# Kernel tuning notes

Hardware: AMD Instinct MI355X
Metric: run time of the kernel (lower is better)

The kernel has to match this reference:

```python
import jax, jax.numpy as jnp
import numpy as np

LN_EPS = 1e-5

def layer_norm(x, gamma, beta):
    mu = jnp.mean(x, axis=-1, keepdims=True)
    var = jnp.mean(jnp.square(x - mu), axis=-1, keepdims=True)
    return (x - mu) * jax.lax.rsqrt(var + LN_EPS) * gamma + beta

def setup_inputs() -> dict:
    key = jax.random.key(0)
    ks = jax.random.split(key, 16)
    B, S, E, D, H, F = 4, 2048, 768, 768, 12, 3072
    dh = D // H
    sc = lambda fan_in: 1.0 / np.sqrt(fan_in)
    x = jax.random.normal(ks[0], (B, S, E), dtype=jnp.float32)
    mask = jax.random.randint(ks[1], (B, S, S), 0, 2) > 0
    # per-head projection weights, torch Linear layout [out, in]
    Wq = jax.random.uniform(ks[2], (H, dh, E), minval=-sc(E), maxval=sc(E))
    bq = jax.random.uniform(ks[3], (H, dh), minval=-sc(E), maxval=sc(E))
    Wk = jax.random.uniform(ks[4], (H, dh, E), minval=-sc(E), maxval=sc(E))
    bk = jax.random.uniform(ks[5], (H, dh), minval=-sc(E), maxval=sc(E))
    Wv = jax.random.uniform(ks[6], (H, dh, E), minval=-sc(E), maxval=sc(E))
    bv = jax.random.uniform(ks[7], (H, dh), minval=-sc(E), maxval=sc(E))
    gamma = jnp.ones((D,), dtype=jnp.float32)
    beta = jnp.zeros((D,), dtype=jnp.float32)
    W1 = jax.random.uniform(ks[8], (F, D), minval=-sc(D), maxval=sc(D))
    b1 = jax.random.uniform(ks[9], (F,), minval=-sc(D), maxval=sc(D))
    W2 = jax.random.uniform(ks[10], (D, F), minval=-sc(F), maxval=sc(F))
    b2 = jax.random.uniform(ks[11], (D,), minval=-sc(F), maxval=sc(F))
    return {"x": x, "mask": mask, "Wq": Wq, "bq": bq, "Wk": Wk, "bk": bk,
            "Wv": Wv, "bv": bv, "gamma": gamma, "beta": beta,
            "W1": W1, "b1": b1, "W2": W2, "b2": b2}

def reference(x, mask, Wq, bq, Wk, bk, Wv, bv, gamma, beta, W1, b1, W2, b2):
    B, S, E = x.shape
    # per-head projections, vectorized over heads: [B,H,S,dh]
    q = jnp.einsum('bse,hde->bhsd', x, Wq) + bq[None, :, None, :]
    k = jnp.einsum('bse,hde->bhsd', x, Wk) + bk[None, :, None, :]
    v = jnp.einsum('bse,hde->bhsd', x, Wv) + bv[None, :, None, :]
    # NOTE: original scales by len(q[0])**0.5 == sqrt(seq_len), not sqrt(d_head)
    scores = jnp.einsum('bhsd,bhtd->bhst', q, k) / jnp.sqrt(jnp.asarray(S, x.dtype))
    scores = jnp.where(mask[:, None, :, :], jnp.asarray(-1000.0, x.dtype), scores)
    # NOTE: original softmax is over dim=1 of [B,Sq,Sk] => the QUERY axis (axis 2 here)
    attn = jax.nn.softmax(scores, axis=2)
    o = jnp.einsum('bhst,bhtd->bhsd', attn, v)  # [B,H,S,dh]
    a = jnp.transpose(o, (0, 2, 1, 3)).reshape(B, S, -1)  # concat heads -> [B,S,D]
    a = layer_norm(a, gamma, beta) + a
    h = jax.nn.relu(jnp.einsum('bsd,fd->bsf', a, W1) + b1)
    b = jnp.einsum('bsf,df->bsd', h, W2) + b2
    b = layer_norm(b, gamma, beta) + b
    return b
```

## Files before the change

kernel.cpp:

```cpp
#include <hip/hip_runtime.h>
#include <hip/hip_bf16.h>
#include <stdint.h>

using bf16 = __hip_bfloat16;
typedef __attribute__((ext_vector_type(8))) short short8;
typedef __attribute__((ext_vector_type(4))) short short4v;
typedef __attribute__((ext_vector_type(4))) float f32x4;

#define MFMA16(a, b, c) __builtin_amdgcn_mfma_f32_16x16x32_bf16((a), (b), (c), 0, 0, 0)

#if __has_builtin(__builtin_amdgcn_mfma_f32_16x16x16bf16_1k)
#define MFMAK16(a, b, c) __builtin_amdgcn_mfma_f32_16x16x16bf16_1k((a), (b), (c), 0, 0, 0)
#elif __has_builtin(__builtin_amdgcn_mfma_f32_16x16x16_bf16_1k)
#define MFMAK16(a, b, c) __builtin_amdgcn_mfma_f32_16x16x16_bf16_1k((a), (b), (c), 0, 0, 0)
#elif __has_builtin(__builtin_amdgcn_mfma_f32_16x16x16_bf16)
#define MFMAK16(a, b, c) __builtin_amdgcn_mfma_f32_16x16x16_bf16((a), (b), (c), 0, 0, 0)
#else
static __device__ __forceinline__ f32x4 mfmak16_asm(short4v a, short4v b, f32x4 c) {
  f32x4 d;
  asm("v_mfma_f32_16x16x16_bf16 %0, %1, %2, %3" : "=v"(d) : "v"(a), "v"(b), "v"(c));
  return d;
}
#define MFMAK16(a, b, c) mfmak16_asm((a), (b), (c))
#endif

static constexpr float SCLE = 0.031879358f;

__device__ __forceinline__ void g2l16(const void* g, void* l) {
  __builtin_amdgcn_global_load_lds((const __attribute__((address_space(1))) void*)g,
                                   (__attribute__((address_space(3))) void*)l, 16, 0, 0);
}

__device__ __forceinline__ short8 frag(const bf16* lds, int row, int slot) {
  return *(const short8*)((const char*)lds + row * 128 + (((slot ^ (row & 7)) & 7) << 4));
}

__global__ __launch_bounds__(256) void cvt_kernel(const float* __restrict__ in,
                                                  bf16* __restrict__ out, int n8) {
  int i = blockIdx.x * 256 + threadIdx.x;
  if (i >= n8) return;
  float4 f0 = ((const float4*)in)[i * 2 + 0];
  float4 f1 = ((const float4*)in)[i * 2 + 1];
  bf16 t[8] = {__float2bfloat16(f0.x), __float2bfloat16(f0.y),
               __float2bfloat16(f0.z), __float2bfloat16(f0.w),
               __float2bfloat16(f1.x), __float2bfloat16(f1.y),
               __float2bfloat16(f1.z), __float2bfloat16(f1.w)};
  ((float4*)out)[i] = *(const float4*)t;
}

__global__ void detect_kernel(const int* __restrict__ m, int* __restrict__ flag) {
  int v = m[threadIdx.x];
  unsigned long long ok = __ballot((v == 0) || (v == 1));
  if (threadIdx.x == 0) *flag = (ok == 0xFFFFFFFFFFFFFFFFULL) ? 1 : 0;
}

__global__ __launch_bounds__(256) void pack_kernel(const void* __restrict__ maskp,
                                                   const int* __restrict__ flagp,
                                                   uint32_t* __restrict__ pm) {
  const int i = blockIdx.x * 256 + threadIdx.x;
  uint32_t nib;
  if (*flagp) {
    const int4 v = ((const int4*)maskp)[i];
    nib = (v.x != 0) | ((v.y != 0) << 1) | ((v.z != 0) << 2) | ((v.w != 0) << 3);
  } else {
    const uchar4 c = ((const uchar4*)maskp)[i];
    nib = (c.x != 0) | ((c.y != 0) << 1) | ((c.z != 0) << 2) | ((c.w != 0) << 3);
  }
  uint32_t w = nib << ((i & 7) * 4);
  w |= __shfl_xor(w, 1, 64);
  w |= __shfl_xor(w, 2, 64);
  w |= __shfl_xor(w, 4, 64);
  if ((threadIdx.x & 7) == 0) pm[i >> 3] = w;
}

template <int EPI>
__global__ __launch_bounds__(256) void gemm_bt_kernel(
    const bf16* __restrict__ A, const bf16* __restrict__ Bm, int N, int K,
    const float* __restrict__ bias0, const float* __restrict__ bias1,
    const float* __restrict__ bias2, void* __restrict__ outp) {
  __shared__ bf16 aLds[2][128 * 32];
  __shared__ bf16 bLds[2][128 * 32];
  const int tid = threadIdx.x;
  const int wave = tid >> 6, lane = tid & 63;
  const int l15 = lane & 15, l4 = lane >> 4;
  const int row0 = blockIdx.y << 7, col0 = blockIdx.x << 7;
  const int wm = (wave >> 1) << 6, wn = (wave & 1) << 6;

  f32x4 acc[4][4] = {};

  const int sr = tid >> 2;
  const int sc = (tid & 3) << 3;
  const bf16* ga = A + (size_t)(row0 + sr) * K + sc;
  const bf16* gb = Bm + (size_t)(col0 + sr) * K + sc;
  const size_t rK64 = (size_t)64 * K;

  auto stage = [&](int buf, int k0) {
    g2l16(ga + k0, &aLds[buf][wave * 512]);
    g2l16(ga + k0 + rK64, &aLds[buf][2048 + wave * 512]);
    g2l16(gb + k0, &bLds[buf][wave * 512]);
    g2l16(gb + k0 + rK64, &bLds[buf][2048 + wave * 512]);
  };

  stage(0, 0);
  __syncthreads();
  const int NT = K >> 5;
  for (int t = 0; t < NT; t++) {
    if (t + 1 < NT) stage((t + 1) & 1, (t + 1) << 5);
    const bf16* la = aLds[t & 1];
    const bf16* lb = bLds[t & 1];
    short8 af[4], bfr[4];
#pragma unroll
    for (int i = 0; i < 4; i++)
      af[i] = *(const short8*)&la[(wm + i * 16 + l15) * 32 + l4 * 8];
#pragma unroll
    for (int i = 0; i < 4; i++)
      bfr[i] = *(const short8*)&lb[(wn + i * 16 + l15) * 32 + l4 * 8];
#pragma unroll
    for (int i = 0; i < 4; i++)
#pragma unroll
      for (int j = 0; j < 4; j++) acc[i][j] = MFMA16(af[i], bfr[j], acc[i][j]);
    __syncthreads();
  }

  if (EPI == 0) {
#pragma unroll
    for (int j = 0; j < 4; j++) {
      const int gcol = col0 + wn + j * 16 + l15;
      const int which = gcol / 768;
      const int oo = gcol - which * 768;
      const float* bs = (which == 0) ? bias0 : ((which == 1) ? bias1 : bias2);
      const float bv = bs[oo];
      const int h = oo >> 6, d = oo & 63;
      if (which < 2) {
        const float scl = (which == 0) ? SCLE : 1.0f;
        bf16* outb = (bf16*)outp + (size_t)which * 6291456;
#pragma unroll
        for (int i = 0; i < 4; i++) {
#pragma unroll
          for (int r = 0; r < 4; r++) {
            const int grow = row0 + wm + i * 16 + l4 * 4 + r;
            const int b = grow >> 11, s = grow & 2047;
            outb[((size_t)((b * 12 + h) * 2048 + s)) * 64 + d] =
                __float2bfloat16((acc[i][j][r] + bv) * scl);
          }
        }
      } else {
        bf16* vt = (bf16*)outp + (size_t)2 * 6291456;
#pragma unroll
        for (int i = 0; i < 4; i++) {
          const int grow = row0 + wm + i * 16 + l4 * 4;
          const int b = grow >> 11, s = grow & 2047;
          bf16 t4[4];
#pragma unroll
          for (int r = 0; r < 4; r++) t4[r] = __float2bfloat16(acc[i][j][r] + bv);
          *(short4v*)&vt[((size_t)((b * 12 + h) * 64 + d)) * 2048 + s] =
              *(const short4v*)t4;
        }
      }
    }
  } else if (EPI == 1) {
    bf16* outb = (bf16*)outp;
#pragma unroll
    for (int j = 0; j < 4; j++) {
      const int gcol = col0 + wn + j * 16 + l15;
      const float bv = bias0[gcol];
#pragma unroll
      for (int i = 0; i < 4; i++)
#pragma unroll
        for (int r = 0; r < 4; r++) {
          const int grow = row0 + wm + i * 16 + l4 * 4 + r;
          float v = acc[i][j][r] + bv;
          v = v > 0.f ? v : 0.f;
          outb[(size_t)grow * N + gcol] = __float2bfloat16(v);
        }
    }
  } else {
    float* outf = (float*)outp;
#pragma unroll
    for (int j = 0; j < 4; j++) {
      const int gcol = col0 + wn + j * 16 + l15;
      const float bv = bias0[gcol];
#pragma unroll
      for (int i = 0; i < 4; i++)
#pragma unroll
        for (int r = 0; r < 4; r++) {
          const int grow = row0 + wm + i * 16 + l4 * 4 + r;
          outf[(size_t)grow * N + gcol] = acc[i][j][r] + bv;
        }
    }
  }
}

__global__ __launch_bounds__(256) void gemm_bt64_kernel(
    const bf16* __restrict__ A, const bf16* __restrict__ Bm, int N, int K,
    const float* __restrict__ bias0, float* __restrict__ outf) {
  __shared__ bf16 aLds[2][64 * 32];
  __shared__ bf16 bLds[2][128 * 32];
  const int tid = threadIdx.x;
  const int wave = tid >> 6, lane = tid & 63;
  const int l15 = lane & 15, l4 = lane >> 4;
  const int row0 = blockIdx.y << 6, col0 = blockIdx.x << 7;
  const int wm = (wave >> 1) << 5, wn = (wave & 1) << 6;

  f32x4 acc[2][4] = {};

  const int sr = tid >> 2;
  const int sc = (tid & 3) << 3;
  const bf16* ga = A + (size_t)(row0 + sr) * K + sc;
  const bf16* gb = Bm + (size_t)(col0 + sr) * K + sc;
  const size_t rK64 = (size_t)64 * K;

  auto stage = [&](int buf, int k0) {
    g2l16(ga + k0, &aLds[buf][wave * 512]);
    g2l16(gb + k0, &bLds[buf][wave * 512]);
    g2l16(gb + k0 + rK64, &bLds[buf][2048 + wave * 512]);
  };

  stage(0, 0);
  __syncthreads();
  const int NT = K >> 5;
  for (int t = 0; t < NT; t++) {
    if (t + 1 < NT) stage((t + 1) & 1, (t + 1) << 5);
    const bf16* la = aLds[t & 1];
    const bf16* lb = bLds[t & 1];
    short8 af[2], bfr[4];
#pragma unroll
    for (int i = 0; i < 2; i++)
      af[i] = *(const short8*)&la[(wm + i * 16 + l15) * 32 + l4 * 8];
#pragma unroll
    for (int j = 0; j < 4; j++)
      bfr[j] = *(const short8*)&lb[(wn + j * 16 + l15) * 32 + l4 * 8];
#pragma unroll
    for (int i = 0; i < 2; i++)
#pragma unroll
      for (int j = 0; j < 4; j++) acc[i][j] = MFMA16(af[i], bfr[j], acc[i][j]);
    __syncthreads();
  }

#pragma unroll
  for (int j = 0; j < 4; j++) {
    const int gcol = col0 + wn + j * 16 + l15;
    const float bv = bias0[gcol];
#pragma unroll
    for (int i = 0; i < 2; i++)
#pragma unroll
      for (int r = 0; r < 4; r++) {
        const int grow = row0 + wm + i * 16 + l4 * 4 + r;
        outf[(size_t)grow * N + gcol] = acc[i][j][r] + bv;
      }
  }
}

__global__ __launch_bounds__(256) void zsum_kernel(
    const bf16* __restrict__ Qb, const bf16* __restrict__ Kb,
    const uint32_t* __restrict__ pm, bf16* __restrict__ Vt) {
  __shared__ bf16 qLds[2][64 * 64];
  __shared__ float zbuf[64];
  const int tid = threadIdx.x, wave = tid >> 6, lane = tid & 63;
  const int l15 = lane & 15, l4 = lane >> 4;
  const int srr = lane >> 3, sss = lane & 7;
  const int bid = blockIdx.x;
  const int swz = (bid & 7) * 192 + (bid >> 3);
  const int bh = swz >> 5, ttile = swz & 31;
  const int b = bh / 12;
  const int t0 = (ttile << 6) + (wave << 4);
  const size_t qkBase = (size_t)bh * (2048 * 64);
  const bf16* Kp = Kb + qkBase;
  const bf16* Qp = Qb + qkBase;
  const uint32_t* pmB = pm + (size_t)b * 2048 * 64;
  const int widx = t0 >> 5;
  const int shft = (wave & 1) * 16 + l4 * 4;

  short8 ak[2];
#pragma unroll
  for (int kc = 0; kc < 2; kc++)
    ak[kc] = *(const short8*)(Kp + (size_t)(t0 + l15) * 64 + kc * 32 + l4 * 8);

  auto stageQ = [&](int buf, int s0) {
#pragma unroll
    for (int p = 0; p < 2; p++) {
      const int r = p * 32 + wave * 8 + srr;
      g2l16(Qp + (size_t)(s0 + r) * 64 + ((sss ^ (r & 7)) << 3),
            &qLds[buf][p * 2048 + wave * 512]);
    }
  };

  f32x4 z = {};
  stageQ(0, 0);
  __syncthreads();

  for (int i = 0; i < 32; i++) {
    const int s0 = i << 6;
    if (i < 31) stageQ((i + 1) & 1, s0 + 64);
    const bf16* qb = qLds[i & 1];
    uint32_t mw[4];
#pragma unroll
    for (int sf = 0; sf < 4; sf++)
      mw[sf] = pmB[(size_t)(s0 + sf * 16 + l15) * 64 + widx];
#pragma unroll
    for (int sf = 0; sf < 4; sf++) {
      const short8 q0 = frag(qb, sf * 16 + l15, l4);
      const short8 q1 = frag(qb, sf * 16 + l15, 4 + l4);
      __builtin_amdgcn_s_setprio(1);
      f32x4 cc = {};
      cc = MFMA16(ak[0], q0, cc);
      cc = MFMA16(ak[1], q1, cc);
      __builtin_amdgcn_s_setprio(0);
      const uint32_t bits = mw[sf] >> shft;
#pragma unroll
      for (int r = 0; r < 4; r++) {
        const float e = __builtin_amdgcn_exp2f(cc[r]);
        z[r] += ((bits >> r) & 1) ? 0.f : e;
      }
    }
    __syncthreads();
  }

#pragma unroll
  for (int r = 0; r < 4; r++) {
    float zz = z[r];
    zz += __shfl_xor(zz, 1, 64);
    zz += __shfl_xor(zz, 2, 64);
    zz += __shfl_xor(zz, 4, 64);
    zz += __shfl_xor(zz, 8, 64);
    if (l15 == 0) zbuf[(wave << 4) + (l4 << 2) + r] = 1.0f / zz;
  }
  __syncthreads();

  const int t0blk = ttile << 6;
  const int drow = tid >> 2;
  const int tcol = (tid & 3) << 4;
  bf16* vp = Vt + (size_t)bh * (64 * 2048) + (size_t)drow * 2048 + t0blk + tcol;
  bf16 v[16];
  *(short8*)&v[0] = *(const short8*)vp;
  *(short8*)&v[8] = *(const short8*)(vp + 8);
#pragma unroll
  for (int j = 0; j < 16; j++)
    v[j] = __float2bfloat16(__bfloat162float(v[j]) * zbuf[tcol + j]);
  *(short8*)vp = *(const short8*)&v[0];
  *(short8*)(vp + 8) = *(const short8*)&v[8];
}

__global__ __launch_bounds__(256, 4) void attn_pv_kernel(
    const bf16* __restrict__ Qb, const bf16* __restrict__ Kb,
    const bf16* __restrict__ Vt, const uint32_t* __restrict__ pm,
    float* __restrict__ aOut) {
  __shared__ bf16 kLds[2][64 * 64];
  __shared__ bf16 vLds[2][64 * 64];
  const int tid = threadIdx.x, wave = tid >> 6, lane = tid & 63;
  const int l15 = lane & 15, l4 = lane >> 4;
  const int srr = lane >> 3, sss = lane & 7;
  const int bid = blockIdx.x;
  const int swz = (bid & 7) * 96 + (bid >> 3);
  const int bh = swz >> 4, stile = swz & 15;
  const int b = bh / 12, h = bh - b * 12;
  const int s0 = (stile << 7) + (wave << 5);
  const size_t qkBase = (size_t)bh * (2048 * 64);
  const bf16* Kp = Kb + qkBase;
  const bf16* Qp = Qb + qkBase;
  const bf16* Vp = Vt + (size_t)bh * 64 * 2048;
  const uint32_t* pmB = pm + (size_t)b * 2048 * 64;

  auto stageKV = [&](int buf, int t0) {
#pragma unroll
    for (int p = 0; p < 2; p++) {
      const int r = p * 32 + wave * 8 + srr;
      g2l16(Kp + (size_t)(t0 + r) * 64 + ((sss ^ (r & 7)) << 3),
            &kLds[buf][p * 2048 + wave * 512]);
      g2l16(Vp + (size_t)r * 2048 + t0 + ((sss ^ (r & 7)) << 3),
            &vLds[buf][p * 2048 + wave * 512]);
    }
  };

  short8 qf[2][2];
#pragma unroll
  for (int mf = 0; mf < 2; mf++)
#pragma unroll
    for (int kc = 0; kc < 2; kc++)
      qf[mf][kc] = *(const short8*)(Qp + (size_t)(s0 + mf * 16 + l15) * 64 +
                                    kc * 32 + l4 * 8);

  f32x4 oacc[2][4] = {};
  stageKV(0, 0);
  __syncthreads();

  for (int i = 0; i < 32; i++) {
    const int t0 = i << 6;
    if (i < 31) stageKV((i + 1) & 1, t0 + 64);
    const bf16* kb = kLds[i & 1];
    const bf16* vb = vLds[i & 1];
    uint2 mw[2];
#pragma unroll
    for (int mf = 0; mf < 2; mf++)
      mw[mf] = *(const uint2*)(pmB + (size_t)(s0 + mf * 16 + l15) * 64 + (t0 >> 5));

#pragma unroll
    for (int tf = 0; tf < 4; tf++) {
      const int trow = tf * 16 + l15;
      const short8 a0 = frag(kb, trow, l4);
      const short8 a1 = frag(kb, trow, 4 + l4);
      short4v pa[2];
#pragma unroll
      for (int mf = 0; mf < 2; mf++) {
        __builtin_amdgcn_s_setprio(1);
        f32x4 cc = {};
        cc = MFMA16(a0, qf[mf][0], cc);
        cc = MFMA16(a1, qf[mf][1], cc);
        __builtin_amdgcn_s_setprio(0);
        const uint32_t bits =
            ((tf < 2) ? mw[mf].x : mw[mf].y) >> ((tf & 1) * 16 + l4 * 4);
        bf16 p4[4];
#pragma unroll
        for (int r = 0; r < 4; r++) {
          const float e = __builtin_amdgcn_exp2f(cc[r]);
          p4[r] = __float2bfloat16(((bits >> r) & 1) ? 0.f : e);
        }
        pa[mf] = *(const short4v*)p4;
      }
      __builtin_amdgcn_s_setprio(1);
#pragma unroll
      for (int nf = 0; nf < 4; nf++) {
        const int vrow = nf * 16 + l15;
        const short4v bv = *(const short4v*)(
            (const char*)vb + vrow * 128 +
            ((((tf * 2 + (l4 >> 1)) ^ (vrow & 7)) & 7) << 4) + (l4 & 1) * 8);
        oacc[0][nf] = MFMAK16(pa[0], bv, oacc[0][nf]);
        oacc[1][nf] = MFMAK16(pa[1], bv, oacc[1][nf]);
      }
      __builtin_amdgcn_s_setprio(0);
    }
    __syncthreads();
  }

#pragma unroll
  for (int mf = 0; mf < 2; mf++)
#pragma unroll
    for (int nf = 0; nf < 4; nf++)
#pragma unroll
      for (int r = 0; r < 4; r++) {
        const int sg = s0 + mf * 16 + l4 * 4 + r;
        const int d = nf * 16 + l15;
        aOut[((size_t)(b * 2048 + sg)) * 768 + h * 64 + d] = oacc[mf][nf][r];
      }
}

template <int OUTMODE>
__global__ __launch_bounds__(256) void ln_kernel(const float* __restrict__ in,
                                                 const float* __restrict__ gamma,
                                                 const float* __restrict__ beta,
                                                 void* __restrict__ outp) {
  const int row = blockIdx.x, tid = threadIdx.x;
  const float* x = in + (size_t)row * 768;
  float v0 = x[tid], v1 = x[tid + 256], v2 = x[tid + 512];
  float s = v0 + v1 + v2;
#pragma unroll
  for (int m = 32; m >= 1; m >>= 1) s += __shfl_xor(s, m, 64);
  __shared__ float red[4];
  if ((tid & 63) == 0) red[tid >> 6] = s;
  __syncthreads();
  s = red[0] + red[1] + red[2] + red[3];
  const float mu = s * (1.f / 768.f);
  const float d0 = v0 - mu, d1 = v1 - mu, d2 = v2 - mu;
  float q = d0 * d0 + d1 * d1 + d2 * d2;
#pragma unroll
  for (int m = 32; m >= 1; m >>= 1) q += __shfl_xor(q, m, 64);
  __syncthreads();
  if ((tid & 63) == 0) red[tid >> 6] = q;
  __syncthreads();
  q = red[0] + red[1] + red[2] + red[3];
  const float rs = rsqrtf(q * (1.f / 768.f) + 1e-5f);
  const float y0 = d0 * rs * gamma[tid] + beta[tid] + v0;
  const float y1 = d1 * rs * gamma[tid + 256] + beta[tid + 256] + v1;
  const float y2 = d2 * rs * gamma[tid + 512] + beta[tid + 512] + v2;
  if (OUTMODE == 0) {
    float* o = (float*)outp + (size_t)row * 768;
    o[tid] = y0; o[tid + 256] = y1; o[tid + 512] = y2;
  } else {
    bf16* o = (bf16*)outp + (size_t)row * 768;
    o[tid] = __float2bfloat16(y0);
    o[tid + 256] = __float2bfloat16(y1);
    o[tid + 512] = __float2bfloat16(y2);
  }
}

extern "C" void kernel_launch(void* const* d_in, const int* in_sizes, int n_in,
                              void* d_out, int out_size, void* d_ws, size_t ws_size,
                              hipStream_t stream) {
  const float* x = (const float*)d_in[0];
  const void* mask = d_in[1];
  const float* Wq = (const float*)d_in[2];
  const float* bq = (const float*)d_in[3];
  const float* Wk = (const float*)d_in[4];
  const float* bk = (const float*)d_in[5];
  const float* Wv = (const float*)d_in[6];
  const float* bv = (const float*)d_in[7];
  const float* gamma = (const float*)d_in[8];
  const float* beta = (const float*)d_in[9];
  const float* W1 = (const float*)d_in[10];
  const float* b1 = (const float*)d_in[11];
  const float* W2 = (const float*)d_in[12];
  const float* b2 = (const float*)d_in[13];
  float* out = (float*)d_out;

  char* ws = (char*)d_ws;
  size_t o = 0;
  auto al = [&](size_t n) { size_t r = o; o = (o + n + 255) & ~(size_t)255; return r; };
  const size_t Q_off = al(12582912);
  const size_t K_off = al(12582912);
  const size_t V_off = al(12582912);
  const size_t XB_off = al(12582912);
  const size_t WQKV_off = al(3538944);
  const size_t H_off = Q_off;
  const size_t W1B_off = al(4718592);
  const size_t W2B_off = al(4718592);
  const size_t A_off = al(25165824);
  const size_t BF_off = A_off;
  const size_t A2_off = al(12582912);
  const size_t FL_off = al(256);
  const size_t PM_off = al(2097152);
  if (o > ws_size) return;

  bf16* Qb = (bf16*)(ws + Q_off);
  bf16* Kb = (bf16*)(ws + K_off);
  bf16* Vt = (bf16*)(ws + V_off);
  bf16* XB = (bf16*)(ws + XB_off);
  bf16* WQKV = (bf16*)(ws + WQKV_off);
  bf16* Hb = (bf16*)(ws + H_off);
  bf16* W1B = (bf16*)(ws + W1B_off);
  bf16* W2B = (bf16*)(ws + W2B_off);
  float* Af = (float*)(ws + A_off);
  float* Bf = (float*)(ws + BF_off);
  bf16* A2b = (bf16*)(ws + A2_off);
  int* flag = (int*)(ws + FL_off);
  uint32_t* pm = (uint32_t*)(ws + PM_off);

  cvt_kernel<<<3072, 256, 0, stream>>>(x, XB, 786432);
  cvt_kernel<<<288, 256, 0, stream>>>(Wq, WQKV, 73728);
  cvt_kernel<<<288, 256, 0, stream>>>(Wk, WQKV + 589824, 73728);
  cvt_kernel<<<288, 256, 0, stream>>>(Wv, WQKV + 2 * 589824, 73728);
  cvt_kernel<<<1152, 256, 0, stream>>>(W1, W1B, 294912);
  cvt_kernel<<<1152, 256, 0, stream>>>(W2, W2B, 294912);
  detect_kernel<<<1, 64, 0, stream>>>((const int*)mask, flag);
  pack_kernel<<<16384, 256, 0, stream>>>(mask, flag, pm);

  gemm_bt_kernel<0><<<dim3(18, 64), 256, 0, stream>>>(XB, WQKV, 2304, 768, bq, bk, bv, Qb);
  zsum_kernel<<<1536, 256, 0, stream>>>(Qb, Kb, pm, Vt);
  attn_pv_kernel<<<768, 256, 0, stream>>>(Qb, Kb, Vt, pm, Af);
  ln_kernel<1><<<8192, 256, 0, stream>>>(Af, gamma, beta, A2b);
  gemm_bt_kernel<1><<<dim3(24, 64), 256, 0, stream>>>(A2b, W1B, 3072, 768, b1, nullptr, nullptr, Hb);
  gemm_bt64_kernel<<<dim3(6, 128), 256, 0, stream>>>(Hb, W2B, 768, 3072, b2, Bf);
  ln_kernel<0><<<8192, 256, 0, stream>>>(Bf, gamma, beta, out);
}
```

Measured before the change: 566.3 us.

## Double key tile per zsum block and read a transposed packed mask

```diff
diff --git a/kernel.cpp b/kernel.cpp
--- a/kernel.cpp
+++ b/kernel.cpp
@@ -56,7 +56,8 @@
 
 __global__ __launch_bounds__(256) void pack_kernel(const void* __restrict__ maskp,
                                                    const int* __restrict__ flagp,
-                                                   uint32_t* __restrict__ pm) {
+                                                   uint32_t* __restrict__ pm,
+                                                   uint32_t* __restrict__ pmT) {
   const int i = blockIdx.x * 256 + threadIdx.x;
   uint32_t nib;
   if (*flagp) {
@@ -70,7 +71,14 @@
   w |= __shfl_xor(w, 1, 64);
   w |= __shfl_xor(w, 2, 64);
   w |= __shfl_xor(w, 4, 64);
-  if ((threadIdx.x & 7) == 0) pm[i >> 3] = w;
+  if ((threadIdx.x & 7) == 0) {
+    const int iw = i >> 3;
+    pm[iw] = w;
+    const int b = iw >> 17;
+    const int rem = iw & 131071;
+    const int s = rem >> 6, tw = rem & 63;
+    pmT[b * 131072 + tw * 2048 + s] = w;
+  }
 }
 
 template <int EPI>
@@ -251,30 +259,31 @@
   }
 }
 
-__global__ __launch_bounds__(256) void zsum_kernel(
+__global__ __launch_bounds__(256, 3) void zsum_kernel(
     const bf16* __restrict__ Qb, const bf16* __restrict__ Kb,
-    const uint32_t* __restrict__ pm, bf16* __restrict__ Vt) {
+    const uint32_t* __restrict__ pmT, bf16* __restrict__ Vt) {
   __shared__ bf16 qLds[2][64 * 64];
-  __shared__ float zbuf[64];
+  __shared__ float zbuf[128];
   const int tid = threadIdx.x, wave = tid >> 6, lane = tid & 63;
   const int l15 = lane & 15, l4 = lane >> 4;
   const int srr = lane >> 3, sss = lane & 7;
   const int bid = blockIdx.x;
-  const int swz = (bid & 7) * 192 + (bid >> 3);
-  const int bh = swz >> 5, ttile = swz & 31;
+  const int swz = (bid & 7) * 96 + (bid >> 3);
+  const int bh = swz >> 4, ttile = swz & 15;
   const int b = bh / 12;
-  const int t0 = (ttile << 6) + (wave << 4);
+  const int t0 = (ttile << 7) + (wave << 5);
   const size_t qkBase = (size_t)bh * (2048 * 64);
   const bf16* Kp = Kb + qkBase;
   const bf16* Qp = Qb + qkBase;
-  const uint32_t* pmB = pm + (size_t)b * 2048 * 64;
-  const int widx = t0 >> 5;
-  const int shft = (wave & 1) * 16 + l4 * 4;
-
-  short8 ak[2];
-#pragma unroll
-  for (int kc = 0; kc < 2; kc++)
-    ak[kc] = *(const short8*)(Kp + (size_t)(t0 + l15) * 64 + kc * 32 + l4 * 8);
+  const uint32_t* pmW = pmT + (size_t)b * 131072 + (size_t)(t0 >> 5) * 2048;
+
+  short8 ak[2][2];
+#pragma unroll
+  for (int tf = 0; tf < 2; tf++)
+#pragma unroll
+    for (int kc = 0; kc < 2; kc++)
+      ak[tf][kc] = *(const short8*)(Kp + (size_t)(t0 + tf * 16 + l15) * 64 +
+                                    kc * 32 + l4 * 8);
 
   auto stageQ = [&](int buf, int s0) {
 #pragma unroll
@@ -285,7 +294,7 @@
     }
   };
 
-  f32x4 z = {};
+  f32x4 z[2] = {};
   stageQ(0, 0);
   __syncthreads();
 
@@ -295,50 +304,55 @@
     const bf16* qb = qLds[i & 1];
     uint32_t mw[4];
 #pragma unroll
-    for (int sf = 0; sf < 4; sf++)
-      mw[sf] = pmB[(size_t)(s0 + sf * 16 + l15) * 64 + widx];
+    for (int sf = 0; sf < 4; sf++) mw[sf] = pmW[s0 + sf * 16 + l15];
 #pragma unroll
     for (int sf = 0; sf < 4; sf++) {
       const short8 q0 = frag(qb, sf * 16 + l15, l4);
       const short8 q1 = frag(qb, sf * 16 + l15, 4 + l4);
-      __builtin_amdgcn_s_setprio(1);
-      f32x4 cc = {};
-      cc = MFMA16(ak[0], q0, cc);
-      cc = MFMA16(ak[1], q1, cc);
-      __builtin_amdgcn_s_setprio(0);
-      const uint32_t bits = mw[sf] >> shft;
-#pragma unroll
-      for (int r = 0; r < 4; r++) {
-        const float e = __builtin_amdgcn_exp2f(cc[r]);
-        z[r] += ((bits >> r) & 1) ? 0.f : e;
+#pragma unroll
+      for (int tf = 0; tf < 2; tf++) {
+        __builtin_amdgcn_s_setprio(1);
+        f32x4 cc = {};
+        cc = MFMA16(ak[tf][0], q0, cc);
+        cc = MFMA16(ak[tf][1], q1, cc);
+        __builtin_amdgcn_s_setprio(0);
+        const uint32_t bits = mw[sf] >> (tf * 16 + l4 * 4);
+#pragma unroll
+        for (int r = 0; r < 4; r++) {
+          const float e = __builtin_amdgcn_exp2f(cc[r]);
+          z[tf][r] += ((bits >> r) & 1) ? 0.f : e;
+        }
       }
     }
     __syncthreads();
   }
 
 #pragma unroll
-  for (int r = 0; r < 4; r++) {
-    float zz = z[r];
-    zz += __shfl_xor(zz, 1, 64);
-    zz += __shfl_xor(zz, 2, 64);
-    zz += __shfl_xor(zz, 4, 64);
-    zz += __shfl_xor(zz, 8, 64);
-    if (l15 == 0) zbuf[(wave << 4) + (l4 << 2) + r] = 1.0f / zz;
-  }
-  __syncthreads();
-
-  const int t0blk = ttile << 6;
+  for (int tf = 0; tf < 2; tf++)
+#pragma unroll
+    for (int r = 0; r < 4; r++) {
+      float zz = z[tf][r];
+      zz += __shfl_xor(zz, 1, 64);
+      zz += __shfl_xor(zz, 2, 64);
+      zz += __shfl_xor(zz, 4, 64);
+      zz += __shfl_xor(zz, 8, 64);
+      if (l15 == 0) zbuf[(wave << 5) + (tf << 4) + (l4 << 2) + r] = 1.0f / zz;
+    }
+  __syncthreads();
+
+  const int tBase = ttile << 7;
   const int drow = tid >> 2;
-  const int tcol = (tid & 3) << 4;
-  bf16* vp = Vt + (size_t)bh * (64 * 2048) + (size_t)drow * 2048 + t0blk + tcol;
-  bf16 v[16];
-  *(short8*)&v[0] = *(const short8*)vp;
-  *(short8*)&v[8] = *(const short8*)(vp + 8);
-#pragma unroll
-  for (int j = 0; j < 16; j++)
-    v[j] = __float2bfloat16(__bfloat162float(v[j]) * zbuf[tcol + j]);
-  *(short8*)vp = *(const short8*)&v[0];
-  *(short8*)(vp + 8) = *(const short8*)&v[8];
+  const int tcol = (tid & 3) << 5;
+  bf16* vp = Vt + (size_t)bh * (64 * 2048) + (size_t)drow * 2048 + tBase + tcol;
+#pragma unroll
+  for (int c = 0; c < 4; c++) {
+    bf16 v[8];
+    *(short8*)v = *(const short8*)(vp + c * 8);
+#pragma unroll
+    for (int j = 0; j < 8; j++)
+      v[j] = __float2bfloat16(__bfloat162float(v[j]) * zbuf[tcol + c * 8 + j]);
+    *(short8*)(vp + c * 8) = *(const short8*)v;
+  }
 }
 
 __global__ __launch_bounds__(256, 4) void attn_pv_kernel(
@@ -438,7 +452,7 @@
     for (int nf = 0; nf < 4; nf++)
 #pragma unroll
       for (int r = 0; r < 4; r++) {
-        const int sg = s0 + mf * 16 + l4 * 4 + r;
+        const int sg = s0 + wave * 0 + mf * 16 + l4 * 4 + r;
         const int d = nf * 16 + l15;
         aOut[((size_t)(b * 2048 + sg)) * 768 + h * 64 + d] = oacc[mf][nf][r];
       }
@@ -518,6 +532,7 @@
   const size_t A2_off = al(12582912);
   const size_t FL_off = al(256);
   const size_t PM_off = al(2097152);
+  const size_t PMT_off = al(2097152);
   if (o > ws_size) return;
 
   bf16* Qb = (bf16*)(ws + Q_off);
@@ -533,6 +548,7 @@
   bf16* A2b = (bf16*)(ws + A2_off);
   int* flag = (int*)(ws + FL_off);
   uint32_t* pm = (uint32_t*)(ws + PM_off);
+  uint32_t* pmT = (uint32_t*)(ws + PMT_off);
 
   cvt_kernel<<<3072, 256, 0, stream>>>(x, XB, 786432);
   cvt_kernel<<<288, 256, 0, stream>>>(Wq, WQKV, 73728);
@@ -541,10 +557,10 @@
   cvt_kernel<<<1152, 256, 0, stream>>>(W1, W1B, 294912);
   cvt_kernel<<<1152, 256, 0, stream>>>(W2, W2B, 294912);
   detect_kernel<<<1, 64, 0, stream>>>((const int*)mask, flag);
-  pack_kernel<<<16384, 256, 0, stream>>>(mask, flag, pm);
+  pack_kernel<<<16384, 256, 0, stream>>>(mask, flag, pm, pmT);
 
   gemm_bt_kernel<0><<<dim3(18, 64), 256, 0, stream>>>(XB, WQKV, 2304, 768, bq, bk, bv, Qb);
-  zsum_kernel<<<1536, 256, 0, stream>>>(Qb, Kb, pm, Vt);
+  zsum_kernel<<<768, 256, 0, stream>>>(Qb, Kb, pmT, Vt);
   attn_pv_kernel<<<768, 256, 0, stream>>>(Qb, Kb, Vt, pm, Af);
   ln_kernel<1><<<8192, 256, 0, stream>>>(Af, gamma, beta, A2b);
   gemm_bt_kernel<1><<<dim3(24, 64), 256, 0, stream>>>(A2b, W1B, 3072, 768, b1, nullptr, nullptr, Hb);
```

Measured after the change: 519.3 us. 8.3% less time.
